# Kernel tuning notes

Hardware: AMD Instinct MI355X
Metric: run time of the kernel (lower is better)

## Reference

```python
import jax, jax.numpy as jnp
import numpy as np

ROWS, COLS = 1024, 1024
N_NODES = ROWS * COLS
RHO_W = 1000.0      # water density
RHO_I = 917.0       # ice density (unused in output path, kept for fidelity)
GRAV = 9.81
SEC_PER_A = 31556926.0
FLOW_COEFF = 0.0405
FLOW_EXP = 1.25     # 5/4
N_ITERS = 32        # fixed-point iterations for MFD flow accumulation


def _raster_links(rows, cols):
    ids = np.arange(rows * cols, dtype=np.int32).reshape(rows, cols)
    src_h = ids[:, :-1].ravel(); dst_h = ids[:, 1:].ravel()
    src_v = ids[:-1, :].ravel(); dst_v = ids[1:, :].ravel()
    return (np.concatenate([src_h, src_v]), np.concatenate([dst_h, dst_v]))


def setup_inputs() -> dict:
    key = jax.random.key(0)
    k1, k2, k3, k4 = jax.random.split(key, 4)
    melt_rate = jax.random.uniform(k1, (N_NODES,), jnp.float32) * 10.0          # m/a
    bedrock_elevation = jax.random.normal(k2, (N_NODES,), jnp.float32) * 500.0  # m
    water_pressure = jax.random.uniform(k3, (N_NODES,), jnp.float32) * 1.0e6    # Pa
    cell_area = jnp.full((N_NODES,), 1.0e4, jnp.float32)                        # 100m cells
    conduit_size = jax.random.uniform(k4, (N_NODES,), jnp.float32) + 0.01
    # landlab-style status: 0 = core node, 1 = fixed-value boundary (perimeter)
    status = np.zeros((ROWS, COLS), dtype=np.int32)
    status[0, :] = 1; status[-1, :] = 1; status[:, 0] = 1; status[:, -1] = 1
    src, dst = _raster_links(ROWS, COLS)
    return {
        "melt_rate": melt_rate,
        "bedrock_elevation": bedrock_elevation,
        "water_pressure": water_pressure,
        "cell_area": cell_area,
        "conduit_size": conduit_size,
        "status_at_node": jnp.asarray(status.ravel()),
        "link_src": jnp.asarray(src),
        "link_dst": jnp.asarray(dst),
    }


def reference(melt_rate, bedrock_elevation, water_pressure, cell_area,
              conduit_size, status_at_node, link_src, link_dst):
    n = melt_rate.shape[0]
    seg = lambda d, i: jax.ops.segment_sum(d, i, num_segments=n)

    # hydraulic potential (surface FlowDirectorMFD routes on)
    phi = RHO_W * GRAV * bedrock_elevation + water_pressure
    # local runoff input at each node
    runoff = melt_rate * cell_area / SEC_PER_A

    # MFD: split each node's outflow among downslope neighbors, proportional
    # to the positive potential drop along each link (unit link length).
    core = (status_at_node == 0)
    dphi = phi[link_src] - phi[link_dst]
    drop_fwd = jnp.maximum(dphi, 0.0) * core[link_src]   # src -> dst
    drop_bwd = jnp.maximum(-dphi, 0.0) * core[link_dst]  # dst -> src
    total_drop = seg(drop_fwd, link_src) + seg(drop_bwd, link_dst)
    s_safe = jnp.where(total_drop > 0.0, total_drop, 1.0)
    frac_fwd = drop_fwd / s_safe[link_src]
    frac_bwd = drop_bwd / s_safe[link_dst]

    # flow accumulation on the drainage DAG: Q = runoff + P^T Q (fixed-point)
    def step(q, _):
        inflow = seg(frac_fwd * q[link_src], link_dst) + seg(frac_bwd * q[link_dst], link_src)
        return runoff + inflow, None

    discharge, _ = jax.lax.scan(step, runoff, None, length=N_ITERS)

    # calc_hydraulic_gradient, masked to core nodes (status == 0)
    gradient = (discharge * FLOW_COEFF * conduit_size ** FLOW_EXP) ** 2
    return jnp.where(status_at_node == 0, gradient, 0.0)
```

## Files before the change

kernel.cpp:

```cpp
#include <hip/hip_runtime.h>

#define ROWS 1024
#define COLS 1024
#define NN (ROWS*COLS)

#define TILE_H 32
#define TILE_W 64
#define HALO   8
#define RH     48
#define RW     80
#define RC     (RH*RW)
#define SPR    (RW/4)
#define NSTRIP (RC/4)
#define NT     256
#define BR     (RH/4)
#define BC     (RW/4)
#define NB4    (BR*BC)

static constexpr float RHOG    = 1000.0f * 9.81f;
static constexpr float INV_SEC = 1.0f / 31556926.0f;
static constexpr float FLOWC   = 0.0405f;

__device__ __forceinline__ float4 gld4(const float* __restrict__ p, int g, bool in) {
    if (in) return *reinterpret_cast<const float4*>(p + g);
    return make_float4(0.f, 0.f, 0.f, 0.f);
}

__global__ __launch_bounds__(256) void k_pre(
        const float* __restrict__ bed, const float* __restrict__ pw,
        const int* __restrict__ status,
        const float* __restrict__ melt, const float* __restrict__ area,
        float* __restrict__ phi, float* __restrict__ inv,
        float* __restrict__ runoff) {
    int i = blockIdx.x * 256 + threadIdx.x;
    int r = i >> 10, c = i & (COLS - 1);
    float p = RHOG * bed[i] + pw[i];
    float t = 0.f;
    if (c > 0)        t += fmaxf(p - (RHOG * bed[i - 1]    + pw[i - 1]),    0.f);
    if (c < COLS - 1) t += fmaxf(p - (RHOG * bed[i + 1]    + pw[i + 1]),    0.f);
    if (r > 0)        t += fmaxf(p - (RHOG * bed[i - COLS] + pw[i - COLS]), 0.f);
    if (r < ROWS - 1) t += fmaxf(p - (RHOG * bed[i + COLS] + pw[i + COLS]), 0.f);
    phi[i]    = p;
    inv[i]    = (status[i] == 0 && t > 0.f) ? (1.f / t) : 0.f;
    runoff[i] = melt[i] * area[i] * INV_SEC;
}

template <bool FIRST, bool FINAL>
__global__ __launch_bounds__(256) void k_fused(
        const float* __restrict__ phi_g, const float* __restrict__ inv_g,
        const float* __restrict__ run_g, const float* __restrict__ qin,
        float* __restrict__ qout,
        const float* __restrict__ cond, const int* __restrict__ status) {
    __shared__ float A[RC];
    __shared__ float Bv[RC];
    __shared__ float4 plT[2][NB4], plB[2][NB4];
    __shared__ float4 plL[2][NB4], plR[2][NB4];
    const int tid = threadIdx.x;
    const int r0 = (int)blockIdx.y * TILE_H - HALO;
    const int c0 = (int)blockIdx.x * TILE_W - HALO;

#pragma unroll
    for (int k = 0; k < 4; ++k) {
        int sidx = tid + k * NT;
        if (sidx < NSTRIP) {
            int sr = sidx / SPR, sc4 = (sidx - sr * SPR) * 4;
            int gr = r0 + sr, gc = c0 + sc4;
            bool in = (gr >= 0) & (gr < ROWS) & (gc >= 0) & (gc < COLS);
            int g = gr * COLS + gc;
            *reinterpret_cast<float4*>(&A[sr * RW + sc4])  = gld4(phi_g, g, in);
            *reinterpret_cast<float4*>(&Bv[sr * RW + sc4]) = gld4(inv_g, g, in);
        }
    }
    __syncthreads();

    const bool active = (tid < NB4);
    const int br = tid / BC, bc = tid - (tid / BC) * BC;
    const int rr0 = 4 * br, cc0 = 4 * bc;
    const bool inter = (br >= 2) & (br <= BR - 3) & (bc >= 2) & (bc <= BC - 3);

    float wW[4][4], wE[4][4], wN[4][4], wS[4][4];
    float q[4][4], ro[4][4];
    int dd[4][4];

    if (active) {
#pragma unroll
        for (int i = 0; i < 4; ++i) {
            int rr = rr0 + i;
            int x = rr * RW + cc0;
            float4 pc = *reinterpret_cast<const float4*>(&A[x]);
            float4 ic = *reinterpret_cast<const float4*>(&Bv[x]);
            int xu = (rr > 0)      ? x - RW : x;
            int xd = (rr < RH - 1) ? x + RW : x;
            float4 pu = *reinterpret_cast<const float4*>(&A[xu]);
            float4 iu = *reinterpret_cast<const float4*>(&Bv[xu]);
            float4 pd = *reinterpret_cast<const float4*>(&A[xd]);
            float4 id = *reinterpret_cast<const float4*>(&Bv[xd]);
            float pl = (cc0 > 0)      ? A[x - 1]  : pc.x;
            float il = (cc0 > 0)      ? Bv[x - 1] : 0.f;
            float pr = (cc0 < RW - 4) ? A[x + 4]  : pc.w;
            float ir = (cc0 < RW - 4) ? Bv[x + 4] : 0.f;
            wN[i][0] = fmaxf(pu.x - pc.x, 0.f) * iu.x;
            wN[i][1] = fmaxf(pu.y - pc.y, 0.f) * iu.y;
            wN[i][2] = fmaxf(pu.z - pc.z, 0.f) * iu.z;
            wN[i][3] = fmaxf(pu.w - pc.w, 0.f) * iu.w;
            wS[i][0] = fmaxf(pd.x - pc.x, 0.f) * id.x;
            wS[i][1] = fmaxf(pd.y - pc.y, 0.f) * id.y;
            wS[i][2] = fmaxf(pd.z - pc.z, 0.f) * id.z;
            wS[i][3] = fmaxf(pd.w - pc.w, 0.f) * id.w;
            wW[i][0] = fmaxf(pl   - pc.x, 0.f) * il;
            wW[i][1] = fmaxf(pc.x - pc.y, 0.f) * ic.x;
            wW[i][2] = fmaxf(pc.y - pc.z, 0.f) * ic.y;
            wW[i][3] = fmaxf(pc.z - pc.w, 0.f) * ic.z;
            wE[i][0] = fmaxf(pc.y - pc.x, 0.f) * ic.y;
            wE[i][1] = fmaxf(pc.z - pc.y, 0.f) * ic.z;
            wE[i][2] = fmaxf(pc.w - pc.z, 0.f) * ic.w;
            wE[i][3] = fmaxf(pr   - pc.w, 0.f) * ir;
        }
#pragma unroll
        for (int i = 0; i < 4; ++i)
#pragma unroll
            for (int j = 0; j < 4; ++j) {
                int rr = rr0 + i, cc = cc0 + j;
                dd[i][j] = min(min(rr, RH - 1 - rr), min(cc, RW - 1 - cc));
            }
#pragma unroll
        for (int i = 0; i < 4; ++i) {
            int gr = r0 + rr0 + i, gc = c0 + cc0;
            bool in = (gr >= 0) & (gr < ROWS) & (gc >= 0) & (gc < COLS);
            int g = gr * COLS + gc;
            float4 r4 = gld4(run_g, g, in);
            ro[i][0] = r4.x; ro[i][1] = r4.y; ro[i][2] = r4.z; ro[i][3] = r4.w;
            float4 q4 = FIRST ? r4 : gld4(qin, g, in);
            q[i][0] = q4.x; q[i][1] = q4.y; q[i][2] = q4.z; q[i][3] = q4.w;
        }
        plT[0][tid] = make_float4(q[0][0], q[0][1], q[0][2], q[0][3]);
        plB[0][tid] = make_float4(q[3][0], q[3][1], q[3][2], q[3][3]);
        plL[0][tid] = make_float4(q[0][0], q[1][0], q[2][0], q[3][0]);
        plR[0][tid] = make_float4(q[0][3], q[1][3], q[2][3], q[3][3]);
    }
    __syncthreads();

    for (int s = 0; s < HALO; ++s) {
        const int pp = s & 1, pn = pp ^ 1;
        if (active) {
            float4 up = plB[pp][(br > 0)      ? tid - BC : tid];
            float4 dn = plT[pp][(br < BR - 1) ? tid + BC : tid];
            float4 lf = plR[pp][(bc > 0)      ? tid - 1  : tid];
            float4 rt = plL[pp][(bc < BC - 1) ? tid + 1  : tid];
            float upv[4] = {up.x, up.y, up.z, up.w};
            float dnv[4] = {dn.x, dn.y, dn.z, dn.w};
            float lfv[4] = {lf.x, lf.y, lf.z, lf.w};
            float rtv[4] = {rt.x, rt.y, rt.z, rt.w};
            float nq[4][4];
#pragma unroll
            for (int i = 0; i < 4; ++i)
#pragma unroll
                for (int j = 0; j < 4; ++j) {
                    float uv = (i > 0) ? q[i - 1][j] : upv[j];
                    float dv = (i < 3) ? q[i + 1][j] : dnv[j];
                    float lv = (j > 0) ? q[i][j - 1] : lfv[i];
                    float rv = (j < 3) ? q[i][j + 1] : rtv[i];
                    float a = ro[i][j];
                    a = fmaf(wW[i][j], lv, a);
                    a = fmaf(wE[i][j], rv, a);
                    a = fmaf(wN[i][j], uv, a);
                    a = fmaf(wS[i][j], dv, a);
                    nq[i][j] = a;
                }
            if (!inter) {
#pragma unroll
                for (int i = 0; i < 4; ++i)
#pragma unroll
                    for (int j = 0; j < 4; ++j)
                        nq[i][j] = (s < dd[i][j]) ? nq[i][j] : q[i][j];
            }
#pragma unroll
            for (int i = 0; i < 4; ++i)
#pragma unroll
                for (int j = 0; j < 4; ++j) q[i][j] = nq[i][j];
            plT[pn][tid] = make_float4(q[0][0], q[0][1], q[0][2], q[0][3]);
            plB[pn][tid] = make_float4(q[3][0], q[3][1], q[3][2], q[3][3]);
            plL[pn][tid] = make_float4(q[0][0], q[1][0], q[2][0], q[3][0]);
            plR[pn][tid] = make_float4(q[0][3], q[1][3], q[2][3], q[3][3]);
        }
        __syncthreads();
    }

    if (active && inter) {
#pragma unroll
        for (int i = 0; i < 4; ++i) {
            int g = (r0 + rr0 + i) * COLS + (c0 + cc0);
            if (FINAL) {
                float4 c4 = *reinterpret_cast<const float4*>(cond + g);
                int4 st   = *reinterpret_cast<const int4*>(status + g);
                float4 o;
                float t;
                t = q[i][0] * FLOWC * (c4.x * sqrtf(sqrtf(c4.x))); o.x = (st.x == 0) ? t * t : 0.f;
                t = q[i][1] * FLOWC * (c4.y * sqrtf(sqrtf(c4.y))); o.y = (st.y == 0) ? t * t : 0.f;
                t = q[i][2] * FLOWC * (c4.z * sqrtf(sqrtf(c4.z))); o.z = (st.z == 0) ? t * t : 0.f;
                t = q[i][3] * FLOWC * (c4.w * sqrtf(sqrtf(c4.w))); o.w = (st.w == 0) ? t * t : 0.f;
                *reinterpret_cast<float4*>(qout + g) = o;
            } else {
                *reinterpret_cast<float4*>(qout + g) =
                    make_float4(q[i][0], q[i][1], q[i][2], q[i][3]);
            }
        }
    }
}

extern "C" void kernel_launch(void* const* d_in, const int* in_sizes, int n_in,
                              void* d_out, int out_size, void* d_ws, size_t ws_size,
                              hipStream_t stream) {
    const float* melt   = (const float*)d_in[0];
    const float* bed    = (const float*)d_in[1];
    const float* pw     = (const float*)d_in[2];
    const float* area   = (const float*)d_in[3];
    const float* cond   = (const float*)d_in[4];
    const int*   status = (const int*)d_in[5];
    float* out = (float*)d_out;

    char* ws = (char*)d_ws;
    float* phi    = (float*)(ws);
    float* inv    = (float*)(ws + 4ull  * NN);
    float* runoff = (float*)(ws + 8ull  * NN);
    float* qA     = (float*)(ws + 12ull * NN);
    float* qB     = (float*)(ws + 16ull * NN);

    k_pre<<<dim3(NN / 256), dim3(256), 0, stream>>>(bed, pw, status, melt, area,
                                                    phi, inv, runoff);

    dim3 grid(COLS / TILE_W, ROWS / TILE_H), block(NT);
    k_fused<true,  false><<<grid, block, 0, stream>>>(phi, inv, runoff, runoff, qA, nullptr, nullptr);
    k_fused<false, false><<<grid, block, 0, stream>>>(phi, inv, runoff, qA, qB, nullptr, nullptr);
    k_fused<false, false><<<grid, block, 0, stream>>>(phi, inv, runoff, qB, qA, nullptr, nullptr);
    k_fused<false, true ><<<grid, block, 0, stream>>>(phi, inv, runoff, qA, out, cond, status);
}
```

Before: 141.3 us.

## Double halo depth to 16 and halve the number of fused iteration launches

Each fused launch now does 16 Jacobi steps on a 64x32 interior tile with a 16-cell halo (96x64 region, 384 threads), so only 2 launches are needed instead of 4. The phi/inv staging buffers and the ping-pong boundary planes now share one aliased shared-memory buffer to fit the larger tile, with an extra barrier before the planes overwrite it. The goal is fewer global round trips of q and fewer launches, paid for with much more redundant halo computation (about 3x the interior area) and longer per-block serial step chains.

```diff
diff --git a/kernel.cpp b/kernel.cpp
--- a/kernel.cpp
+++ b/kernel.cpp
@@ -4,18 +4,17 @@
 #define COLS 1024
 #define NN (ROWS*COLS)
 
-#define TILE_H 32
-#define TILE_W 64
-#define HALO   8
-#define RH     48
-#define RW     80
+#define TILE_H 64
+#define TILE_W 32
+#define HALO   16
+#define RH     96
+#define RW     64
 #define RC     (RH*RW)
 #define SPR    (RW/4)
 #define NSTRIP (RC/4)
-#define NT     256
+#define NT     384
 #define BR     (RH/4)
 #define BC     (RW/4)
-#define NB4    (BR*BC)
 
 static constexpr float RHOG    = 1000.0f * 9.81f;
 static constexpr float INV_SEC = 1.0f / 31556926.0f;
@@ -46,15 +45,19 @@
 }
 
 template <bool FIRST, bool FINAL>
-__global__ __launch_bounds__(256) void k_fused(
+__global__ __launch_bounds__(NT) void k_fused(
         const float* __restrict__ phi_g, const float* __restrict__ inv_g,
         const float* __restrict__ run_g, const float* __restrict__ qin,
         float* __restrict__ qout,
         const float* __restrict__ cond, const int* __restrict__ status) {
-    __shared__ float A[RC];
-    __shared__ float Bv[RC];
-    __shared__ float4 plT[2][NB4], plB[2][NB4];
-    __shared__ float4 plL[2][NB4], plR[2][NB4];
+    __shared__ __align__(16) char smem[8 * NT * 16];
+    float*  A   = (float*)smem;
+    float*  Bv  = A + RC;
+    float4* plT = (float4*)smem;
+    float4* plB = plT + 2 * NT;
+    float4* plL = plB + 2 * NT;
+    float4* plR = plL + 2 * NT;
+
     const int tid = threadIdx.x;
     const int r0 = (int)blockIdx.y * TILE_H - HALO;
     const int c0 = (int)blockIdx.x * TILE_W - HALO;
@@ -62,131 +65,127 @@
 #pragma unroll
     for (int k = 0; k < 4; ++k) {
         int sidx = tid + k * NT;
-        if (sidx < NSTRIP) {
-            int sr = sidx / SPR, sc4 = (sidx - sr * SPR) * 4;
-            int gr = r0 + sr, gc = c0 + sc4;
-            bool in = (gr >= 0) & (gr < ROWS) & (gc >= 0) & (gc < COLS);
-            int g = gr * COLS + gc;
-            *reinterpret_cast<float4*>(&A[sr * RW + sc4])  = gld4(phi_g, g, in);
-            *reinterpret_cast<float4*>(&Bv[sr * RW + sc4]) = gld4(inv_g, g, in);
-        }
+        int sr = sidx / SPR, sc4 = (sidx - sr * SPR) * 4;
+        int gr = r0 + sr, gc = c0 + sc4;
+        bool in = (gr >= 0) & (gr < ROWS) & (gc >= 0) & (gc < COLS);
+        int g = gr * COLS + gc;
+        *reinterpret_cast<float4*>(&A[sr * RW + sc4])  = gld4(phi_g, g, in);
+        *reinterpret_cast<float4*>(&Bv[sr * RW + sc4]) = gld4(inv_g, g, in);
     }
     __syncthreads();
 
-    const bool active = (tid < NB4);
     const int br = tid / BC, bc = tid - (tid / BC) * BC;
     const int rr0 = 4 * br, cc0 = 4 * bc;
-    const bool inter = (br >= 2) & (br <= BR - 3) & (bc >= 2) & (bc <= BC - 3);
+    const bool inter = (br >= HALO / 4) & (br < BR - HALO / 4) &
+                       (bc >= HALO / 4) & (bc < BC - HALO / 4);
 
     float wW[4][4], wE[4][4], wN[4][4], wS[4][4];
     float q[4][4], ro[4][4];
     int dd[4][4];
 
-    if (active) {
-#pragma unroll
-        for (int i = 0; i < 4; ++i) {
-            int rr = rr0 + i;
-            int x = rr * RW + cc0;
-            float4 pc = *reinterpret_cast<const float4*>(&A[x]);
-            float4 ic = *reinterpret_cast<const float4*>(&Bv[x]);
-            int xu = (rr > 0)      ? x - RW : x;
-            int xd = (rr < RH - 1) ? x + RW : x;
-            float4 pu = *reinterpret_cast<const float4*>(&A[xu]);
-            float4 iu = *reinterpret_cast<const float4*>(&Bv[xu]);
-            float4 pd = *reinterpret_cast<const float4*>(&A[xd]);
-            float4 id = *reinterpret_cast<const float4*>(&Bv[xd]);
-            float pl = (cc0 > 0)      ? A[x - 1]  : pc.x;
-            float il = (cc0 > 0)      ? Bv[x - 1] : 0.f;
-            float pr = (cc0 < RW - 4) ? A[x + 4]  : pc.w;
-            float ir = (cc0 < RW - 4) ? Bv[x + 4] : 0.f;
-            wN[i][0] = fmaxf(pu.x - pc.x, 0.f) * iu.x;
-            wN[i][1] = fmaxf(pu.y - pc.y, 0.f) * iu.y;
-            wN[i][2] = fmaxf(pu.z - pc.z, 0.f) * iu.z;
-            wN[i][3] = fmaxf(pu.w - pc.w, 0.f) * iu.w;
-            wS[i][0] = fmaxf(pd.x - pc.x, 0.f) * id.x;
-            wS[i][1] = fmaxf(pd.y - pc.y, 0.f) * id.y;
-            wS[i][2] = fmaxf(pd.z - pc.z, 0.f) * id.z;
-            wS[i][3] = fmaxf(pd.w - pc.w, 0.f) * id.w;
-            wW[i][0] = fmaxf(pl   - pc.x, 0.f) * il;
-            wW[i][1] = fmaxf(pc.x - pc.y, 0.f) * ic.x;
-            wW[i][2] = fmaxf(pc.y - pc.z, 0.f) * ic.y;
-            wW[i][3] = fmaxf(pc.z - pc.w, 0.f) * ic.z;
-            wE[i][0] = fmaxf(pc.y - pc.x, 0.f) * ic.y;
-            wE[i][1] = fmaxf(pc.z - pc.y, 0.f) * ic.z;
-            wE[i][2] = fmaxf(pc.w - pc.z, 0.f) * ic.w;
-            wE[i][3] = fmaxf(pr   - pc.w, 0.f) * ir;
+#pragma unroll
+    for (int i = 0; i < 4; ++i) {
+        int rr = rr0 + i;
+        int x = rr * RW + cc0;
+        float4 pc = *reinterpret_cast<const float4*>(&A[x]);
+        float4 ic = *reinterpret_cast<const float4*>(&Bv[x]);
+        int xu = (rr > 0)      ? x - RW : x;
+        int xd = (rr < RH - 1) ? x + RW : x;
+        float4 pu = *reinterpret_cast<const float4*>(&A[xu]);
+        float4 iu = *reinterpret_cast<const float4*>(&Bv[xu]);
+        float4 pd = *reinterpret_cast<const float4*>(&A[xd]);
+        float4 id = *reinterpret_cast<const float4*>(&Bv[xd]);
+        float pl = (cc0 > 0)      ? A[x - 1]  : pc.x;
+        float il = (cc0 > 0)      ? Bv[x - 1] : 0.f;
+        float pr = (cc0 < RW - 4) ? A[x + 4]  : pc.w;
+        float ir = (cc0 < RW - 4) ? Bv[x + 4] : 0.f;
+        wN[i][0] = fmaxf(pu.x - pc.x, 0.f) * iu.x;
+        wN[i][1] = fmaxf(pu.y - pc.y, 0.f) * iu.y;
+        wN[i][2] = fmaxf(pu.z - pc.z, 0.f) * iu.z;
+        wN[i][3] = fmaxf(pu.w - pc.w, 0.f) * iu.w;
+        wS[i][0] = fmaxf(pd.x - pc.x, 0.f) * id.x;
+        wS[i][1] = fmaxf(pd.y - pc.y, 0.f) * id.y;
+        wS[i][2] = fmaxf(pd.z - pc.z, 0.f) * id.z;
+        wS[i][3] = fmaxf(pd.w - pc.w, 0.f) * id.w;
+        wW[i][0] = fmaxf(pl   - pc.x, 0.f) * il;
+        wW[i][1] = fmaxf(pc.x - pc.y, 0.f) * ic.x;
+        wW[i][2] = fmaxf(pc.y - pc.z, 0.f) * ic.y;
+        wW[i][3] = fmaxf(pc.z - pc.w, 0.f) * ic.z;
+        wE[i][0] = fmaxf(pc.y - pc.x, 0.f) * ic.y;
+        wE[i][1] = fmaxf(pc.z - pc.y, 0.f) * ic.z;
+        wE[i][2] = fmaxf(pc.w - pc.z, 0.f) * ic.w;
+        wE[i][3] = fmaxf(pr   - pc.w, 0.f) * ir;
+    }
+#pragma unroll
+    for (int i = 0; i < 4; ++i)
+#pragma unroll
+        for (int j = 0; j < 4; ++j) {
+            int rr = rr0 + i, cc = cc0 + j;
+            dd[i][j] = min(min(rr, RH - 1 - rr), min(cc, RW - 1 - cc));
         }
 #pragma unroll
-        for (int i = 0; i < 4; ++i)
-#pragma unroll
-            for (int j = 0; j < 4; ++j) {
-                int rr = rr0 + i, cc = cc0 + j;
-                dd[i][j] = min(min(rr, RH - 1 - rr), min(cc, RW - 1 - cc));
-            }
-#pragma unroll
-        for (int i = 0; i < 4; ++i) {
-            int gr = r0 + rr0 + i, gc = c0 + cc0;
-            bool in = (gr >= 0) & (gr < ROWS) & (gc >= 0) & (gc < COLS);
-            int g = gr * COLS + gc;
-            float4 r4 = gld4(run_g, g, in);
-            ro[i][0] = r4.x; ro[i][1] = r4.y; ro[i][2] = r4.z; ro[i][3] = r4.w;
-            float4 q4 = FIRST ? r4 : gld4(qin, g, in);
-            q[i][0] = q4.x; q[i][1] = q4.y; q[i][2] = q4.z; q[i][3] = q4.w;
-        }
-        plT[0][tid] = make_float4(q[0][0], q[0][1], q[0][2], q[0][3]);
-        plB[0][tid] = make_float4(q[3][0], q[3][1], q[3][2], q[3][3]);
-        plL[0][tid] = make_float4(q[0][0], q[1][0], q[2][0], q[3][0]);
-        plR[0][tid] = make_float4(q[0][3], q[1][3], q[2][3], q[3][3]);
-    }
+    for (int i = 0; i < 4; ++i) {
+        int gr = r0 + rr0 + i, gc = c0 + cc0;
+        bool in = (gr >= 0) & (gr < ROWS) & (gc >= 0) & (gc < COLS);
+        int g = gr * COLS + gc;
+        float4 r4 = gld4(run_g, g, in);
+        ro[i][0] = r4.x; ro[i][1] = r4.y; ro[i][2] = r4.z; ro[i][3] = r4.w;
+        float4 q4 = FIRST ? r4 : gld4(qin, g, in);
+        q[i][0] = q4.x; q[i][1] = q4.y; q[i][2] = q4.z; q[i][3] = q4.w;
+    }
+    __syncthreads();
+
+    plT[tid]      = make_float4(q[0][0], q[0][1], q[0][2], q[0][3]);
+    plB[tid]      = make_float4(q[3][0], q[3][1], q[3][2], q[3][3]);
+    plL[tid]      = make_float4(q[0][0], q[1][0], q[2][0], q[3][0]);
+    plR[tid]      = make_float4(q[0][3], q[1][3], q[2][3], q[3][3]);
     __syncthreads();
 
     for (int s = 0; s < HALO; ++s) {
         const int pp = s & 1, pn = pp ^ 1;
-        if (active) {
-            float4 up = plB[pp][(br > 0)      ? tid - BC : tid];
-            float4 dn = plT[pp][(br < BR - 1) ? tid + BC : tid];
-            float4 lf = plR[pp][(bc > 0)      ? tid - 1  : tid];
-            float4 rt = plL[pp][(bc < BC - 1) ? tid + 1  : tid];
-            float upv[4] = {up.x, up.y, up.z, up.w};
-            float dnv[4] = {dn.x, dn.y, dn.z, dn.w};
-            float lfv[4] = {lf.x, lf.y, lf.z, lf.w};
-            float rtv[4] = {rt.x, rt.y, rt.z, rt.w};
-            float nq[4][4];
+        float4 up = plB[pp * NT + ((br > 0)      ? tid - BC : tid)];
+        float4 dn = plT[pp * NT + ((br < BR - 1) ? tid + BC : tid)];
+        float4 lf = plR[pp * NT + ((bc > 0)      ? tid - 1  : tid)];
+        float4 rt = plL[pp * NT + ((bc < BC - 1) ? tid + 1  : tid)];
+        float upv[4] = {up.x, up.y, up.z, up.w};
+        float dnv[4] = {dn.x, dn.y, dn.z, dn.w};
+        float lfv[4] = {lf.x, lf.y, lf.z, lf.w};
+        float rtv[4] = {rt.x, rt.y, rt.z, rt.w};
+        float nq[4][4];
+#pragma unroll
+        for (int i = 0; i < 4; ++i)
+#pragma unroll
+            for (int j = 0; j < 4; ++j) {
+                float uv = (i > 0) ? q[i - 1][j] : upv[j];
+                float dv = (i < 3) ? q[i + 1][j] : dnv[j];
+                float lv = (j > 0) ? q[i][j - 1] : lfv[i];
+                float rv = (j < 3) ? q[i][j + 1] : rtv[i];
+                float a = ro[i][j];
+                a = fmaf(wW[i][j], lv, a);
+                a = fmaf(wE[i][j], rv, a);
+                a = fmaf(wN[i][j], uv, a);
+                a = fmaf(wS[i][j], dv, a);
+                nq[i][j] = a;
+            }
+        if (!inter) {
 #pragma unroll
             for (int i = 0; i < 4; ++i)
 #pragma unroll
-                for (int j = 0; j < 4; ++j) {
-                    float uv = (i > 0) ? q[i - 1][j] : upv[j];
-                    float dv = (i < 3) ? q[i + 1][j] : dnv[j];
-                    float lv = (j > 0) ? q[i][j - 1] : lfv[i];
-                    float rv = (j < 3) ? q[i][j + 1] : rtv[i];
-                    float a = ro[i][j];
-                    a = fmaf(wW[i][j], lv, a);
-                    a = fmaf(wE[i][j], rv, a);
-                    a = fmaf(wN[i][j], uv, a);
-                    a = fmaf(wS[i][j], dv, a);
-                    nq[i][j] = a;
-                }
-            if (!inter) {
-#pragma unroll
-                for (int i = 0; i < 4; ++i)
-#pragma unroll
-                    for (int j = 0; j < 4; ++j)
-                        nq[i][j] = (s < dd[i][j]) ? nq[i][j] : q[i][j];
-            }
-#pragma unroll
-            for (int i = 0; i < 4; ++i)
-#pragma unroll
-                for (int j = 0; j < 4; ++j) q[i][j] = nq[i][j];
-            plT[pn][tid] = make_float4(q[0][0], q[0][1], q[0][2], q[0][3]);
-            plB[pn][tid] = make_float4(q[3][0], q[3][1], q[3][2], q[3][3]);
-            plL[pn][tid] = make_float4(q[0][0], q[1][0], q[2][0], q[3][0]);
-            plR[pn][tid] = make_float4(q[0][3], q[1][3], q[2][3], q[3][3]);
+                for (int j = 0; j < 4; ++j)
+                    nq[i][j] = (s < dd[i][j]) ? nq[i][j] : q[i][j];
         }
+#pragma unroll
+        for (int i = 0; i < 4; ++i)
+#pragma unroll
+            for (int j = 0; j < 4; ++j) q[i][j] = nq[i][j];
+        plT[pn * NT + tid] = make_float4(q[0][0], q[0][1], q[0][2], q[0][3]);
+        plB[pn * NT + tid] = make_float4(q[3][0], q[3][1], q[3][2], q[3][3]);
+        plL[pn * NT + tid] = make_float4(q[0][0], q[1][0], q[2][0], q[3][0]);
+        plR[pn * NT + tid] = make_float4(q[0][3], q[1][3], q[2][3], q[3][3]);
         __syncthreads();
     }
 
-    if (active && inter) {
+    if (inter) {
 #pragma unroll
         for (int i = 0; i < 4; ++i) {
             int g = (r0 + rr0 + i) * COLS + (c0 + cc0);
@@ -224,14 +223,11 @@
     float* inv    = (float*)(ws + 4ull  * NN);
     float* runoff = (float*)(ws + 8ull  * NN);
     float* qA     = (float*)(ws + 12ull * NN);
-    float* qB     = (float*)(ws + 16ull * NN);
 
     k_pre<<<dim3(NN / 256), dim3(256), 0, stream>>>(bed, pw, status, melt, area,
                                                     phi, inv, runoff);
 
     dim3 grid(COLS / TILE_W, ROWS / TILE_H), block(NT);
     k_fused<true,  false><<<grid, block, 0, stream>>>(phi, inv, runoff, runoff, qA, nullptr, nullptr);
-    k_fused<false, false><<<grid, block, 0, stream>>>(phi, inv, runoff, qA, qB, nullptr, nullptr);
-    k_fused<false, false><<<grid, block, 0, stream>>>(phi, inv, runoff, qB, qA, nullptr, nullptr);
     k_fused<false, true ><<<grid, block, 0, stream>>>(phi, inv, runoff, qA, out, cond, status);
 }
```

New measurement: 152.7 us. 1.08x slower.
